# Performance work log

Measured on AMD Instinct MI355X. Metric: run time of the kernel, lower is better.

The kernel has to match this reference:

```python
import jax, jax.numpy as jnp
import numpy as np

NUM_EXPERTS = 8
TOP_K = 2
HIDDEN = 1024
NUM_TOKENS = 8192


def setup_inputs() -> dict:
    key = jax.random.key(0)
    k1, k2, k3 = jax.random.split(key, 3)
    x = jax.random.normal(k1, (NUM_TOKENS, HIDDEN), dtype=jnp.float32)
    # gate: nn.Linear(hidden, num_experts, bias=False) -> weight [E, H]
    gate_w = jax.random.normal(k2, (NUM_EXPERTS, HIDDEN), dtype=jnp.float32) * 0.02
    # experts: nn.Linear(hidden, hidden, bias=False) stacked -> [E, H_out, H_in]
    expert_w = jax.random.normal(k3, (NUM_EXPERTS, HIDDEN, HIDDEN), dtype=jnp.float32) * 0.02
    return {"x": x, "gate_w": gate_w, "expert_w": expert_w}


def reference(x, gate_w, expert_w):
    # --- routing ---
    logits = jnp.einsum("th,eh->te", x, gate_w)          # [T, E]
    probs = jax.nn.softmax(logits, axis=-1)
    weights, indices = jax.lax.top_k(probs, TOP_K)        # [T, K], [T, K]

    # --- expert compute (equivalent of dispatch + per-expert GEMM) ---
    # y_e = x @ W_e^T for every expert; tokens then gather their top-k rows.
    all_y = jnp.einsum("td,ehd->eth", x, expert_w)        # [E, T, H]

    # --- weighted combine (gather by routed expert ids) ---
    t_idx = jnp.arange(x.shape[0])[None, :]               # [1, T]
    y_sel = all_y[indices.T, t_idx, :]                    # [K, T, H]
    out = jnp.einsum("tk,kth->th", weights, y_sel)        # [T, H]
    return out
```

## Files before the change

### kernel.cpp

```cpp
#include <hip/hip_runtime.h>
#include <hip/hip_bf16.h>
#include <stdint.h>

#define NUM_TOKENS 8192
#define HIDDEN 1024
#define NEXP 8
#define TOPK 2

typedef __bf16 bf16;
typedef __bf16 bf16x4 __attribute__((ext_vector_type(4)));
typedef __bf16 bf16x8 __attribute__((ext_vector_type(8)));
typedef float f32x4 __attribute__((ext_vector_type(4)));

__device__ __forceinline__ void gld_lds16(const void* g, void* l) {
  __builtin_amdgcn_global_load_lds(
      (const __attribute__((address_space(1))) void*)(uintptr_t)g,
      (__attribute__((address_space(3))) void*)(uint32_t)(uintptr_t)l,
      16, 0, 0);
}

__global__ __launch_bounds__(256) void prep_kernel(
    const float* __restrict__ x, const float* __restrict__ gw,
    const float* __restrict__ ew,
    bf16* __restrict__ xbf, bf16* __restrict__ wbf,
    int* __restrict__ echoice, float* __restrict__ pchoice,
    float* __restrict__ out)
{
  const int b   = blockIdx.x;
  const int tid = threadIdx.x;

  if (b < 2048) {
    const int wid  = tid >> 6;
    const int lane = tid & 63;
    const int t = b * 4 + wid;

    const float* xrow = x + (size_t)t * HIDDEN;
    bf16* xbrow = xbf + (size_t)t * HIDDEN;

    float acc[NEXP];
#pragma unroll
    for (int e = 0; e < NEXP; ++e) acc[e] = 0.f;

#pragma unroll
    for (int it = 0; it < 4; ++it) {
      const int idx = it * 256 + lane * 4;
      float4 xv = *(const float4*)(xrow + idx);
      bf16x4 xb;
      xb[0] = (bf16)xv.x; xb[1] = (bf16)xv.y; xb[2] = (bf16)xv.z; xb[3] = (bf16)xv.w;
      *(bf16x4*)(xbrow + idx) = xb;
#pragma unroll
      for (int e = 0; e < NEXP; ++e) {
        float4 gv = *(const float4*)(gw + e * HIDDEN + idx);
        acc[e] += xv.x * gv.x + xv.y * gv.y + xv.z * gv.z + xv.w * gv.w;
      }
    }
#pragma unroll
    for (int e = 0; e < NEXP; ++e) {
#pragma unroll
      for (int off = 32; off > 0; off >>= 1)
        acc[e] += __shfl_xor(acc[e], off, 64);
    }

    if (lane == 0) {
      float m = acc[0];
#pragma unroll
      for (int e = 1; e < NEXP; ++e) m = fmaxf(m, acc[e]);
      float p[NEXP]; float s = 0.f;
#pragma unroll
      for (int e = 0; e < NEXP; ++e) { p[e] = expf(acc[e] - m); s += p[e]; }
      const float inv = 1.f / s;
#pragma unroll
      for (int e = 0; e < NEXP; ++e) p[e] *= inv;
      int i0 = 0; float p0 = p[0];
#pragma unroll
      for (int e = 1; e < NEXP; ++e) if (p[e] > p0) { p0 = p[e]; i0 = e; }
      int i1 = -1; float p1 = -1.f;
#pragma unroll
      for (int e = 0; e < NEXP; ++e) if (e != i0 && p[e] > p1) { p1 = p[e]; i1 = e; }

      echoice[t]              = i0;
      echoice[NUM_TOKENS + t] = i1;
      pchoice[t]              = p0;
      pchoice[NUM_TOKENS + t] = p1;
    }
  } else if (b < 4096) {
    const size_t i = ((size_t)(b - 2048) * 256 + tid) * 16;
    float4 v0 = *(const float4*)(ew + i);
    float4 v1 = *(const float4*)(ew + i + 4);
    float4 v2 = *(const float4*)(ew + i + 8);
    float4 v3 = *(const float4*)(ew + i + 12);
    bf16x8 o0, o1;
    o0[0] = (bf16)v0.x; o0[1] = (bf16)v0.y; o0[2] = (bf16)v0.z; o0[3] = (bf16)v0.w;
    o0[4] = (bf16)v1.x; o0[5] = (bf16)v1.y; o0[6] = (bf16)v1.z; o0[7] = (bf16)v1.w;
    o1[0] = (bf16)v2.x; o1[1] = (bf16)v2.y; o1[2] = (bf16)v2.z; o1[3] = (bf16)v2.w;
    o1[4] = (bf16)v3.x; o1[5] = (bf16)v3.y; o1[6] = (bf16)v3.z; o1[7] = (bf16)v3.w;
    *(bf16x8*)(wbf + i)     = o0;
    *(bf16x8*)(wbf + i + 8) = o1;
  } else {
    const size_t i = ((size_t)(b - 4096) * 256 + tid) * 16;
    const float4 z = {0.f, 0.f, 0.f, 0.f};
    *(float4*)(out + i)      = z;
    *(float4*)(out + i + 4)  = z;
    *(float4*)(out + i + 8)  = z;
    *(float4*)(out + i + 12) = z;
  }
}

__global__ __launch_bounds__(1024) void build_lists_kernel(
    const int* __restrict__ echoice, const float* __restrict__ pchoice,
    int* __restrict__ cnt, int* __restrict__ tok, float* __restrict__ wt)
{
  const int list = blockIdx.x;
  const int k = list >> 3;
  const int e = list & 7;
  const int tid  = threadIdx.x;
  const int wave = tid >> 6;
  const int lane = tid & 63;
  const int tbase = wave * 512;

  const int*   ec = echoice + k * NUM_TOKENS;
  const float* pc = pchoice + k * NUM_TOKENS;

  __shared__ int wcnt[16];
  __shared__ int woff[16];

  const unsigned long long lower = ((unsigned long long)1 << lane) - 1;

  int   ev[8];
  float pv[8];
#pragma unroll
  for (int c = 0; c < 8; ++c) {
    ev[c] = ec[tbase + c * 64 + lane];
    pv[c] = pc[tbase + c * 64 + lane];
  }
  unsigned long long m[8];
  int cl = 0;
#pragma unroll
  for (int c = 0; c < 8; ++c) { m[c] = __ballot(ev[c] == e); cl += __popcll(m[c]); }
  if (lane == 0) wcnt[wave] = cl;
  __syncthreads();
  if (tid == 0) {
    int off = 0;
#pragma unroll
    for (int w = 0; w < 16; ++w) { woff[w] = off; off += wcnt[w]; }
    cnt[list] = off;
  }
  __syncthreads();
  int run = woff[wave];
#pragma unroll
  for (int c = 0; c < 8; ++c) {
    if (ev[c] == e) {
      const int pos = run + __popcll(m[c] & lower);
      tok[(size_t)list * NUM_TOKENS + pos] = tbase + c * 64 + lane;
      wt [(size_t)list * NUM_TOKENS + pos] = pv[c];
    }
    run += __popcll(m[c]);
  }
}

__global__ __launch_bounds__(512, 2) void moe_gemm_kernel(
    const bf16* __restrict__ xbf, const bf16* __restrict__ wbf,
    const int* __restrict__ cnt, const int* __restrict__ tok,
    const float* __restrict__ wt, float* __restrict__ out)
{
  const int e  = blockIdx.z >> 1;
  const int k  = blockIdx.z & 1;
  const int list = k * NEXP + e;
  const int mt = blockIdx.y;
  const int nt = blockIdx.x;
  const int count = cnt[list];
  const int m0 = mt * 256;
  if (m0 >= count) return;
  const int rows = min(256, count - m0);

  __shared__ __align__(16) bf16 As[4 * 256 * 32];
  __shared__ __align__(16) bf16 Bs[4 * 256 * 32];
  __shared__ int   tok_s[256];
  __shared__ float wt_s[256];

  const int tid = threadIdx.x;
  if (tid < 256) {
    if (tid < rows) {
      tok_s[tid] = tok[(size_t)list * NUM_TOKENS + m0 + tid];
      wt_s[tid]  = wt [(size_t)list * NUM_TOKENS + m0 + tid];
    } else { tok_s[tid] = 0; wt_s[tid] = 0.f; }
  }
  __syncthreads();

  const int csrc = (((tid & 3) ^ ((tid >> 3) & 3)) << 3);
  const int r0 = tid >> 2;
  const bf16* gA0 = xbf + (size_t)tok_s[r0] * HIDDEN + csrc;
  const bf16* gA1 = xbf + (size_t)tok_s[r0 + 128] * HIDDEN + csrc;
  const bf16* gB0 = wbf + (size_t)e * HIDDEN * HIDDEN
                  + (size_t)(nt * 256 + r0) * HIDDEN + csrc;
  const bf16* gB1 = gB0 + (size_t)128 * HIDDEN;

  auto STAGE = [&](int t, int buf) {
    const int kc = t << 5;
    bf16* la = As + buf * 8192 + tid * 8;
    bf16* lb = Bs + buf * 8192 + tid * 8;
    gld_lds16(gA0 + kc, la);
    gld_lds16(gA1 + kc, la + 4096);
    gld_lds16(gB0 + kc, lb);
    gld_lds16(gB1 + kc, lb + 4096);
  };

  const int wid  = tid >> 6;
  const int lane = tid & 63;
  const int wm = (wid >> 2) * 128;
  const int wn = (wid & 3) * 64;
  const int qm = lane & 15;
  const int l4 = lane >> 4;

  f32x4 acc[8][4];
#pragma unroll
  for (int i = 0; i < 8; ++i)
#pragma unroll
    for (int j = 0; j < 4; ++j) acc[i][j] = (f32x4){0.f, 0.f, 0.f, 0.f};

  auto COMPUTE = [&](int buf) {
    const bf16* Ab = As + buf * 8192;
    const bf16* Bb = Bs + buf * 8192;
    bf16x8 a[8], b[4];
#pragma unroll
    for (int i = 0; i < 8; ++i) {
      const int r = wm + i * 16 + qm;
      a[i] = *(const bf16x8*)(Ab + r * 32 + ((l4 ^ ((r >> 1) & 3)) << 3));
    }
#pragma unroll
    for (int j = 0; j < 4; ++j) {
      const int r = wn + j * 16 + qm;
      b[j] = *(const bf16x8*)(Bb + r * 32 + ((l4 ^ ((r >> 1) & 3)) << 3));
    }
    __builtin_amdgcn_s_setprio(1);
#pragma unroll
    for (int i = 0; i < 8; ++i)
#pragma unroll
      for (int j = 0; j < 4; ++j)
        acc[i][j] = __builtin_amdgcn_mfma_f32_16x16x32_bf16(a[i], b[j], acc[i][j], 0, 0, 0);
    __builtin_amdgcn_s_setprio(0);
  };

  STAGE(0, 0); STAGE(1, 1); STAGE(2, 2);

#pragma unroll 1
  for (int t = 0; t < 29; ++t) {
    asm volatile("s_waitcnt vmcnt(8)" ::: "memory");
    __builtin_amdgcn_s_barrier();
    STAGE(t + 3, (t + 3) & 3);
    COMPUTE(t & 3);
  }
  asm volatile("s_waitcnt vmcnt(8)" ::: "memory");
  __builtin_amdgcn_s_barrier();
  COMPUTE(1);
  asm volatile("s_waitcnt vmcnt(4)" ::: "memory");
  __builtin_amdgcn_s_barrier();
  COMPUTE(2);
  asm volatile("s_waitcnt vmcnt(0)" ::: "memory");
  __builtin_amdgcn_s_barrier();
  COMPUTE(3);

  const int h0 = nt * 256 + wn + qm;
#pragma unroll
  for (int i = 0; i < 8; ++i) {
    const int rbase = wm + i * 16 + (lane >> 4) * 4;
#pragma unroll
    for (int r = 0; r < 4; ++r) {
      const int rl = rbase + r;
      if (rl < rows) {
        const int t = tok_s[rl];
        const float w = wt_s[rl];
        float* orow = out + (size_t)t * HIDDEN + h0;
#pragma unroll
        for (int j = 0; j < 4; ++j) {
          const float v = w * acc[i][j][r];
          unsafeAtomicAdd(orow + j * 16, v);
        }
      }
    }
  }
}

extern "C" void kernel_launch(void* const* d_in, const int* in_sizes, int n_in,
                              void* d_out, int out_size, void* d_ws, size_t ws_size,
                              hipStream_t stream) {
  const float* x  = (const float*)d_in[0];
  const float* gw = (const float*)d_in[1];
  const float* ew = (const float*)d_in[2];
  float* out = (float*)d_out;

  char* ws = (char*)d_ws;
  int*   cnt     = (int*)ws;
  int*   echoice = (int*)(ws + 256);
  float* pchoice = (float*)(ws + 256 + (size_t)2 * NUM_TOKENS * 4);
  int*   tok = (int*)(ws + 256 + (size_t)4 * NUM_TOKENS * 4);
  float* wt  = (float*)(ws + 256 + (size_t)20 * NUM_TOKENS * 4);
  bf16*  xbf = (bf16*)(ws + 256 + (size_t)36 * NUM_TOKENS * 4);
  bf16*  wbf = (bf16*)((char*)xbf + (size_t)NUM_TOKENS * HIDDEN * 2);

  prep_kernel<<<6144, 256, 0, stream>>>(x, gw, ew, xbf, wbf, echoice, pchoice, out);
  build_lists_kernel<<<2 * NEXP, 1024, 0, stream>>>(echoice, pchoice, cnt, tok, wt);

  dim3 grid(HIDDEN / 256, NUM_TOKENS / 256, 2 * NEXP);
  moe_gemm_kernel<<<grid, 512, 0, stream>>>(xbf, wbf, cnt, tok, wt, out);
}
```

Baseline: 223.9 us.

## Swizzle MoE GEMM block order and split compute into interleaved half-steps

Block indices are remapped so that blocks landing on the same XCD (flat index mod 8) cover contiguous tiles, aiming to improve L2 reuse of expert weights and gathered token rows. The main loop now splits each k-step into two halves. Each half loads part of the B fragments from LDS, issues half of the global-to-LDS prefetch for the next stage, then runs half of the MFMAs, so memory issue and matrix math interleave more finely. This adds an extra barrier per iteration and a more complex schedule, which may add synchronisation overhead.

Result: faster. 213.4 us (-4.7%).

```diff
diff --git a/kernel.cpp b/kernel.cpp
--- a/kernel.cpp
+++ b/kernel.cpp
@@ -163,11 +163,14 @@
     const int* __restrict__ cnt, const int* __restrict__ tok,
     const float* __restrict__ wt, float* __restrict__ out)
 {
-  const int e  = blockIdx.z >> 1;
-  const int k  = blockIdx.z & 1;
+  const int flat = blockIdx.x + (blockIdx.y << 2) + (blockIdx.z << 7);
+  const int swz  = (flat & 7) * 256 + (flat >> 3);
+  const int nt = swz & 3;
+  const int mt = (swz >> 2) & 31;
+  const int z  = swz >> 7;
+  const int e  = z >> 1;
+  const int k  = z & 1;
   const int list = k * NEXP + e;
-  const int mt = blockIdx.y;
-  const int nt = blockIdx.x;
   const int count = cnt[list];
   const int m0 = mt * 256;
   if (m0 >= count) return;
@@ -195,12 +198,15 @@
                   + (size_t)(nt * 256 + r0) * HIDDEN + csrc;
   const bf16* gB1 = gB0 + (size_t)128 * HIDDEN;
 
-  auto STAGE = [&](int t, int buf) {
+  auto STAGE_A = [&](int t, int buf) {
     const int kc = t << 5;
     bf16* la = As + buf * 8192 + tid * 8;
-    bf16* lb = Bs + buf * 8192 + tid * 8;
     gld_lds16(gA0 + kc, la);
     gld_lds16(gA1 + kc, la + 4096);
+  };
+  auto STAGE_B = [&](int t, int buf) {
+    const int kc = t << 5;
+    bf16* lb = Bs + buf * 8192 + tid * 8;
     gld_lds16(gB0 + kc, lb);
     gld_lds16(gB1 + kc, lb + 4096);
   };
@@ -218,47 +224,68 @@
 #pragma unroll
     for (int j = 0; j < 4; ++j) acc[i][j] = (f32x4){0.f, 0.f, 0.f, 0.f};
 
-  auto COMPUTE = [&](int buf) {
+  bf16x8 a[8], b2[2];
+
+  auto LOAD_A = [&](int buf) {
     const bf16* Ab = As + buf * 8192;
-    const bf16* Bb = Bs + buf * 8192;
-    bf16x8 a[8], b[4];
 #pragma unroll
     for (int i = 0; i < 8; ++i) {
       const int r = wm + i * 16 + qm;
       a[i] = *(const bf16x8*)(Ab + r * 32 + ((l4 ^ ((r >> 1) & 3)) << 3));
     }
-#pragma unroll
-    for (int j = 0; j < 4; ++j) {
-      const int r = wn + j * 16 + qm;
-      b[j] = *(const bf16x8*)(Bb + r * 32 + ((l4 ^ ((r >> 1) & 3)) << 3));
-    }
+  };
+  auto LOAD_B2 = [&](int buf, int j0) {
+    const bf16* Bb = Bs + buf * 8192;
+#pragma unroll
+    for (int j = 0; j < 2; ++j) {
+      const int r = wn + (j0 + j) * 16 + qm;
+      b2[j] = *(const bf16x8*)(Bb + r * 32 + ((l4 ^ ((r >> 1) & 3)) << 3));
+    }
+  };
+  auto MFMA2 = [&](int j0) {
     __builtin_amdgcn_s_setprio(1);
 #pragma unroll
     for (int i = 0; i < 8; ++i)
 #pragma unroll
-      for (int j = 0; j < 4; ++j)
-        acc[i][j] = __builtin_amdgcn_mfma_f32_16x16x32_bf16(a[i], b[j], acc[i][j], 0, 0, 0);
+      for (int j = 0; j < 2; ++j)
+        acc[i][j0 + j] = __builtin_amdgcn_mfma_f32_16x16x32_bf16(a[i], b2[j], acc[i][j0 + j], 0, 0, 0);
     __builtin_amdgcn_s_setprio(0);
   };
 
-  STAGE(0, 0); STAGE(1, 1); STAGE(2, 2);
+  STAGE_A(0, 0); STAGE_B(0, 0);
+  STAGE_A(1, 1); STAGE_B(1, 1);
+  STAGE_A(2, 2); STAGE_B(2, 2);
 
 #pragma unroll 1
   for (int t = 0; t < 29; ++t) {
+    const int c  = t & 3;
+    const int nb = (t + 3) & 3;
     asm volatile("s_waitcnt vmcnt(8)" ::: "memory");
     __builtin_amdgcn_s_barrier();
-    STAGE(t + 3, (t + 3) & 3);
-    COMPUTE(t & 3);
-  }
+    LOAD_A(c);
+    LOAD_B2(c, 0);
+    STAGE_A(t + 3, nb);
+    MFMA2(0);
+    __builtin_amdgcn_s_barrier();
+    LOAD_B2(c, 2);
+    STAGE_B(t + 3, nb);
+    MFMA2(2);
+  }
+  auto TAILSTEP = [&](int buf) {
+    __builtin_amdgcn_s_barrier();
+    LOAD_A(buf);
+    LOAD_B2(buf, 0);
+    MFMA2(0);
+    __builtin_amdgcn_s_barrier();
+    LOAD_B2(buf, 2);
+    MFMA2(2);
+  };
   asm volatile("s_waitcnt vmcnt(8)" ::: "memory");
-  __builtin_amdgcn_s_barrier();
-  COMPUTE(1);
+  TAILSTEP(1);
   asm volatile("s_waitcnt vmcnt(4)" ::: "memory");
-  __builtin_amdgcn_s_barrier();
-  COMPUTE(2);
+  TAILSTEP(2);
   asm volatile("s_waitcnt vmcnt(0)" ::: "memory");
-  __builtin_amdgcn_s_barrier();
-  COMPUTE(3);
+  TAILSTEP(3);
 
   const int h0 = nt * 256 + wn + qm;
 #pragma unroll
```
